# Performance work log

Hardware: AMD Instinct MI355X
Metric: run time of the kernel (lower is better)

Reference implementation:

```python
import jax, jax.numpy as jnp
import numpy as np

B, C, H, W = 4, 64, 128, 128
KS = 3
PAD = 1
N = KS * KS


def conv2d(x, w, b=None, stride=1, padding=0):
    out = jax.lax.conv_general_dilated(
        x, w, (stride, stride), [(padding, padding), (padding, padding)],
        dimension_numbers=("NCHW", "OIHW", "NCHW"))
    if b is not None:
        out = out + b[None, :, None, None]
    return out


def setup_inputs() -> dict:
    key = jax.random.key(0)
    ks = jax.random.split(key, 6)
    scale = 0.05  # small weights so offsets stay in a realistic range
    return {
        "x": jax.random.normal(ks[0], (B, C, H, W), jnp.float32),
        "p_w": jax.random.normal(ks[1], (2 * N, C, 3, 3), jnp.float32) * scale,
        "p_b": jax.random.normal(ks[2], (2 * N,), jnp.float32) * scale,
        "m_w": jax.random.normal(ks[3], (N, C, 3, 3), jnp.float32) * scale,
        "m_b": jax.random.normal(ks[4], (N,), jnp.float32) * scale,
        "conv_w": jax.random.normal(ks[5], (C, C, KS, KS), jnp.float32) * (1.0 / np.sqrt(C * N)),
    }


def reference(x, p_w, p_b, m_w, m_b, conv_w):
    b, c, h, w = x.shape
    # offset / modulation branches (stride=1, padding=1, 3x3)
    offset = conv2d(x, p_w, p_b, 1, 1)                 # (b, 2N, h, w)
    m = jax.nn.sigmoid(conv2d(x, m_w, m_b, 1, 1))      # (b, N,  h, w)

    xp = jnp.pad(x, ((0, 0), (0, 0), (PAD, PAD), (PAD, PAD)))
    Hp, Wp = h + 2 * PAD, w + 2 * PAD

    # sampling positions p = p_0 + p_n + offset, layout (b, h, w, 2N): first N rows(x), last N cols(y)
    pnx, pny = jnp.meshgrid(jnp.arange(-1, 2), jnp.arange(-1, 2), indexing="ij")
    p_n = jnp.concatenate([pnx.ravel(), pny.ravel()]).astype(x.dtype)          # (2N,)
    base_x = jnp.broadcast_to(jnp.arange(1, h + 1)[:, None, None], (h, w, N))
    base_y = jnp.broadcast_to(jnp.arange(1, w + 1)[None, :, None], (h, w, N))
    base = jnp.concatenate([base_x, base_y], axis=-1).astype(x.dtype)          # (h, w, 2N)
    p = jnp.transpose(offset, (0, 2, 3, 1)) + p_n + base[None]                 # (b, h, w, 2N)

    px, py = p[..., :N], p[..., N:]
    # integer corners from detached p (floor), clamped to padded extent
    qf = jnp.floor(jax.lax.stop_gradient(p))
    qx_lt = jnp.clip(qf[..., :N], 0, Hp - 1).astype(jnp.int32)
    qy_lt = jnp.clip(qf[..., N:], 0, Wp - 1).astype(jnp.int32)
    qx_rb = jnp.clip(qf[..., :N] + 1, 0, Hp - 1).astype(jnp.int32)
    qy_rb = jnp.clip(qf[..., N:] + 1, 0, Wp - 1).astype(jnp.int32)

    pxc = jnp.clip(px, 0, Hp - 1)
    pyc = jnp.clip(py, 0, Wp - 1)

    g_lt = (1 + (qx_lt - pxc)) * (1 + (qy_lt - pyc))
    g_rb = (1 - (qx_rb - pxc)) * (1 - (qy_rb - pyc))
    g_lb = (1 + (qx_lt - pxc)) * (1 - (qy_rb - pyc))
    g_rt = (1 - (qx_rb - pxc)) * (1 + (qy_lt - pyc))

    xp_flat = xp.reshape(b, c, Hp * Wp)

    def gather(qx, qy):
        idx = (qx * Wp + qy).reshape(b, -1)                     # (b, h*w*N)
        out = jax.vmap(lambda xf, i: xf[:, i])(xp_flat, idx)    # (b, c, h*w*N)
        return out.reshape(b, c, h, w, N)

    x_off = (g_lt[:, None] * gather(qx_lt, qy_lt)
             + g_rb[:, None] * gather(qx_rb, qy_rb)
             + g_lb[:, None] * gather(qx_lt, qy_rb)
             + g_rt[:, None] * gather(qx_rb, qy_lt))            # (b, c, h, w, N)

    x_off = x_off * jnp.transpose(m, (0, 2, 3, 1))[:, None]     # modulation

    # _reshape_x_offset: n = 3*i + j -> (b, c, h*3, w*3) with layout (h, i, w, j)
    x_off = x_off.reshape(b, c, h, w, KS, KS)
    x_off = jnp.transpose(x_off, (0, 1, 2, 4, 3, 5)).reshape(b, c, h * KS, w * KS)

    return conv2d(x_off, conv_w, None, stride=KS, padding=0)    # (b, outc, h, w)
```

## Files before the change

### kernel.cpp

```cpp
#include <hip/hip_runtime.h>
#include <hip/hip_bf16.h>
#include <math.h>

#define BB 4
#define CC 64
#define HH 128
#define WW 128
#define NPT 9
#define HW (HH*WW)
#define HP 130
#define WP 130

typedef __attribute__((ext_vector_type(8))) short bf16x8;
typedef __attribute__((ext_vector_type(4))) float f32x4;

static __device__ __forceinline__ unsigned short f2bf(float f) {
    __hip_bfloat16 h = __float2bfloat16(f);
    return *reinterpret_cast<unsigned short*>(&h);
}
static __device__ __forceinline__ float bf2f(unsigned short u) {
    return __uint_as_float(((unsigned int)u) << 16);
}

__global__ __launch_bounds__(256) void k_pre(
    const float* __restrict__ x, const float* __restrict__ cw,
    const float* __restrict__ pw, const float* __restrict__ pb,
    const float* __restrict__ mw, const float* __restrict__ mb,
    unsigned short* __restrict__ xt, unsigned short* __restrict__ wtt,
    unsigned short* __restrict__ wttB, float* __restrict__ b27)
{
    __shared__ float tile[64][132];
    int bid = blockIdx.x;
    int t = threadIdx.x;
    if (bid < BB * HH) {
        int b = bid >> 7, h = bid & 127;
        const float* xb = x + ((size_t)b * CC) * HW + h * WW;
        #pragma unroll
        for (int i = 0; i < 8; ++i) {
            int idx = i * 256 + t;
            int ci = idx >> 5, w4 = idx & 31;
            float4 v = *reinterpret_cast<const float4*>(xb + (size_t)ci * HW + w4 * 4);
            *reinterpret_cast<float4*>(&tile[ci][w4 * 4]) = v;
        }
        __syncthreads();
        unsigned short* xtb = xt + (((size_t)b * HP + (h + 1)) * WP + 1) * 64;
        #pragma unroll
        for (int i = 0; i < 4; ++i) {
            int idx = i * 256 + t;
            int w = idx >> 3, cig = idx & 7;
            unsigned int pk[4];
            #pragma unroll
            for (int k = 0; k < 4; ++k) {
                unsigned int u0 = f2bf(tile[cig * 8 + 2 * k][w]);
                unsigned int u1 = f2bf(tile[cig * 8 + 2 * k + 1][w]);
                pk[k] = u0 | (u1 << 16);
            }
            *reinterpret_cast<int4*>(xtb + (size_t)w * 64 + cig * 8) =
                *reinterpret_cast<int4*>(&pk[0]);
        }
        return;
    }
    int i = (bid - BB * HH) * 256 + t;
    if (i < 36864) {
        int cot = i / 9216;
        int rem = i - cot * 9216;
        int n   = rem >> 10;
        int s2  = (rem >> 9) & 1;
        int lhi = (rem >> 7) & 3;
        int l15 = (rem >> 3) & 15;
        int j   = i & 7;
        int co = cot * 16 + l15;
        int ci = s2 * 32 + lhi * 8 + j;
        wtt[i] = f2bf(cw[(co * 64 + ci) * 9 + n]);
    } else if (i < 55296) {
        int q = i - 36864;
        int j   = q & 7;
        int co  = (q >> 3) & 31;
        int lhi = (q >> 8) & 3;
        int s2  = (q >> 10) & 1;
        int n   = q >> 11;
        int ci  = s2 * 32 + lhi * 8 + j;
        float v = 0.f;
        if (co < 18) v = pw[(co * 64 + ci) * 9 + n];
        else if (co < 27) v = mw[((co - 18) * 64 + ci) * 9 + n];
        wttB[q] = f2bf(v);
    } else if (i < 55328) {
        int co = i - 55296;
        b27[co] = (co < 18) ? pb[co] : (co < 27 ? mb[co - 18] : 0.f);
    } else if (i < 55328 + BB * 4128) {
        int p = i - 55328;
        int b = p / 4128, r = p - b * 4128;
        size_t base;
        if (r < 2080) {
            int row = r / 1040;
            int rr  = r - row * 1040;
            int wp = rr >> 3, c8 = rr & 7;
            int hp = row ? (HP - 1) : 0;
            base = (((size_t)b * HP + hp) * WP + wp) * 64 + c8 * 8;
        } else {
            int r2 = r - 2080;
            int col = r2 >> 10;
            int rr  = r2 & 1023;
            int hp = (rr >> 3) + 1, c8 = rr & 7;
            int wp = col ? (WP - 1) : 0;
            base = (((size_t)b * HP + hp) * WP + wp) * 64 + c8 * 8;
        }
        *reinterpret_cast<int4*>(xt + base) = make_int4(0, 0, 0, 0);
    }
}

#define OMS 68
#define NCX 198

union SmemU {
    unsigned short astage[NCX * 64];
    struct {
        int geo[576 * 8];
        union {
            float om[27 * OMS];
            unsigned int xoff[2][2048];
        } u2;
    } d;
};

__global__ __launch_bounds__(512, 4) void k_fused(
    const unsigned short* __restrict__ xt, const unsigned short* __restrict__ wttB,
    const float* __restrict__ b27, const unsigned short* __restrict__ wtt,
    float* __restrict__ out)
{
    __shared__ SmemU su;

    int blk0 = blockIdx.x;
    int blk = (blk0 & 7) * 128 + (blk0 >> 3);
    int wblk = blk & 1;
    int h = (blk >> 1) & 127;
    int b = blk >> 8;
    int w0 = wblk * 64;
    int t = threadIdx.x;
    int ln = t & 63, wid = t >> 6;
    int ln15 = ln & 15, lhi = ln >> 4;

    const unsigned short* xtb = xt + (size_t)b * HP * WP * 64;
    char* astage_c = reinterpret_cast<char*>(su.astage);
    float* s_om = su.d.u2.om;

    for (int uu = t; uu < NCX * 8; uu += 512) {
        int cx = uu >> 3, o16 = uu & 7;
        int r = cx / 66, c = cx - r * 66;
        const unsigned short* src = xtb + ((size_t)(h + r) * WP + (w0 + c)) * 64 + o16 * 8;
        int4 v = *reinterpret_cast<const int4*>(src);
        *reinterpret_cast<int4*>(astage_c + cx * 128 + ((o16 ^ (cx & 7)) << 4)) = v;
    }
    __syncthreads();

    {
        int pxg = wid >> 1, coh = wid & 1;
        int px = pxg * 16 + ln15;
        f32x4 acc;
        acc[0] = 0.f; acc[1] = 0.f; acc[2] = 0.f; acc[3] = 0.f;
        const unsigned short* wB = wttB + (size_t)(coh * 16 + ln15) * 8 + lhi * 256;
        bf16x8 bfc = *reinterpret_cast<const bf16x8*>(wB);
        #pragma unroll
        for (int ns = 0; ns < 18; ++ns) {
            bf16x8 bfn = bfc;
            if (ns < 17)
                bfn = *reinterpret_cast<const bf16x8*>(wB + (size_t)(ns + 1) * 1024);
            int n = ns >> 1, s2 = ns & 1;
            int kh = n / 3, kw = n - kh * 3;
            int cx = kh * 66 + px + kw;
            int o16 = s2 * 4 + lhi;
            bf16x8 af = *reinterpret_cast<const bf16x8*>(
                astage_c + cx * 128 + ((o16 ^ (cx & 7)) << 4));
            acc = __builtin_amdgcn_mfma_f32_16x16x32_bf16(af, bfc, acc, 0, 0, 0);
            bfc = bfn;
        }
        __syncthreads();
        int co = coh * 16 + ln15;
        int prow = pxg * 16 + lhi * 4;
        if (co < 27) {
            float bias = b27[co];
            float4 v;
            v.x = acc[0] + bias; v.y = acc[1] + bias;
            v.z = acc[2] + bias; v.w = acc[3] + bias;
            if (co >= 18) {
                v.x = 1.f / (1.f + expf(-v.x));
                v.y = 1.f / (1.f + expf(-v.y));
                v.z = 1.f / (1.f + expf(-v.z));
                v.w = 1.f / (1.f + expf(-v.w));
            }
            *reinterpret_cast<float4*>(&s_om[co * OMS + prow]) = v;
        }
    }
    __syncthreads();

    int* s_geo = su.d.geo;

    for (int idx = t; idx < NPT * 64; idx += 512) {
        int n = idx >> 6, px = idx & 63;
        float ox = s_om[n * OMS + px];
        float oy = s_om[(9 + n) * OMS + px];
        float mk = s_om[(18 + n) * OMS + px];
        float pxf = ox + (float)(n / 3 - 1) + (float)(h + 1);
        float pyf = oy + (float)(n % 3 - 1) + (float)(w0 + px + 1);
        float fx = floorf(pxf), fy = floorf(pyf);
        int qxlt = (int)fminf(fmaxf(fx, 0.f), 129.f);
        int qylt = (int)fminf(fmaxf(fy, 0.f), 129.f);
        int qxrb = (int)fminf(fmaxf(fx + 1.f, 0.f), 129.f);
        int qyrb = (int)fminf(fmaxf(fy + 1.f, 0.f), 129.f);
        float pxc = fminf(fmaxf(pxf, 0.f), 129.f);
        float pyc = fminf(fmaxf(pyf, 0.f), 129.f);
        float ax = 1.f + (float)qxlt - pxc;
        float bx = 1.f - ((float)qxrb - pxc);
        float ay = 1.f + (float)qylt - pyc;
        float by = 1.f - ((float)qyrb - pyc);
        int* g = &s_geo[idx * 8];
        float4 wv;
        wv.x = ax * ay * mk;
        wv.y = bx * by * mk;
        wv.z = ax * by * mk;
        wv.w = bx * ay * mk;
        int4 av;
        av.x = (qxlt * WP + qylt) * 64;
        av.y = (qxrb * WP + qyrb) * 64;
        av.z = (qxlt * WP + qyrb) * 64;
        av.w = (qxrb * WP + qylt) * 64;
        *reinterpret_cast<float4*>(g) = wv;
        *reinterpret_cast<int4*>(g + 4) = av;
    }
    __syncthreads();

    f32x4 acc[2];
    #pragma unroll
    for (int g = 0; g < 2; ++g) {
        acc[g][0] = 0.f; acc[g][1] = 0.f; acc[g][2] = 0.f; acc[g][3] = 0.f;
    }

    const unsigned short* wbase = wtt + (size_t)(wid & 3) * 9216;
    int px_s = t >> 3;
    int cig_s = t & 7;
    int coff = cig_s * 8;
    char* xoff_base = reinterpret_cast<char*>(su.d.u2.xoff);
    int ghalf = wid >> 2;
    int wsw = (cig_s * 16) ^ ((px_s & 7) << 4);

    bf16x8 ga0, ga1, ga2, ga3, gb0, gb1, gb2, gb3;

#define GATHER(S0, S1, S2, S3, NN) do {                                        \
        const int4 av_ = *reinterpret_cast<const int4*>(                       \
            &s_geo[((NN) * 64 + px_s) * 8] + 4);                               \
        S0 = *reinterpret_cast<const bf16x8*>(xtb + av_.x + coff);             \
        S1 = *reinterpret_cast<const bf16x8*>(xtb + av_.y + coff);             \
        S2 = *reinterpret_cast<const bf16x8*>(xtb + av_.z + coff);             \
        S3 = *reinterpret_cast<const bf16x8*>(xtb + av_.w + coff);             \
    } while (0)

#define PACK(S0, S1, S2, S3, NN) do {                                          \
        const float4 wv_ = *reinterpret_cast<const float4*>(                   \
            &s_geo[((NN) * 64 + px_s) * 8]);                                   \
        unsigned int pk_[4];                                                   \
        _Pragma("unroll")                                                      \
        for (int i_ = 0; i_ < 4; ++i_) {                                       \
            float va_ = wv_.x * bf2f((unsigned short)S0[2*i_])                 \
                      + wv_.y * bf2f((unsigned short)S1[2*i_])                 \
                      + wv_.z * bf2f((unsigned short)S2[2*i_])                 \
                      + wv_.w * bf2f((unsigned short)S3[2*i_]);                \
            float vb_ = wv_.x * bf2f((unsigned short)S0[2*i_+1])               \
                      + wv_.y * bf2f((unsigned short)S1[2*i_+1])               \
                      + wv_.z * bf2f((unsigned short)S2[2*i_+1])               \
                      + wv_.w * bf2f((unsigned short)S3[2*i_+1]);              \
            pk_[i_] = __builtin_amdgcn_perm(__float_as_uint(vb_),              \
                                            __float_as_uint(va_), 0x07060302u); \
        }                                                                      \
        *reinterpret_cast<int4*>(xoff_base + ((NN) & 1) * 8192 + px_s * 128 + wsw) \
            = *reinterpret_cast<int4*>(&pk_[0]);                               \
    } while (0)

#define MFMA_N(NN) do {                                                        \
        bf16x8 bf0_ = *reinterpret_cast<const bf16x8*>(                        \
            wbase + (NN) * 1024 + lhi * 128 + ln15 * 8);                       \
        bf16x8 bf1_ = *reinterpret_cast<const bf16x8*>(                        \
            wbase + (NN) * 1024 + 512 + lhi * 128 + ln15 * 8);                 \
        char* rbuf_ = xoff_base + ((NN) & 1) * 8192;                           \
        _Pragma("unroll")                                                      \
        for (int s2_ = 0; s2_ < 2; ++s2_) {                                    \
            bf16x8 bfr_ = s2_ ? bf1_ : bf0_;                                   \
            _Pragma("unroll")                                                  \
            for (int g_ = 0; g_ < 2; ++g_) {                                   \
                int row_ = (ghalf * 2 + g_) * 16 + ln15;                       \
                int cb2_ = (s2_ * 32 + lhi * 8) * 2;                           \
                bf16x8 af_ = *reinterpret_cast<const bf16x8*>(                 \
                    rbuf_ + row_ * 128 + (cb2_ ^ ((row_ & 7) << 4)));          \
                acc[g_] = __builtin_amdgcn_mfma_f32_16x16x32_bf16(             \
                    af_, bfr_, acc[g_], 0, 0, 0);                              \
            }                                                                  \
        }                                                                      \
    } while (0)

    GATHER(ga0, ga1, ga2, ga3, 0);
    GATHER(gb0, gb1, gb2, gb3, 1);
    PACK(ga0, ga1, ga2, ga3, 0);
    __syncthreads();

#define DSTEP(NN, N0, N1, N2, N3, P0, P1, P2, P3) do {                         \
        if ((NN) + 2 < NPT) GATHER(N0, N1, N2, N3, (NN) + 2);                  \
        MFMA_N(NN);                                                            \
        if ((NN) + 1 < NPT) {                                                  \
            PACK(P0, P1, P2, P3, (NN) + 1);                                    \
            __syncthreads();                                                   \
        }                                                                      \
    } while (0)

    DSTEP(0, ga0, ga1, ga2, ga3, gb0, gb1, gb2, gb3);
    DSTEP(1, gb0, gb1, gb2, gb3, ga0, ga1, ga2, ga3);
    DSTEP(2, ga0, ga1, ga2, ga3, gb0, gb1, gb2, gb3);
    DSTEP(3, gb0, gb1, gb2, gb3, ga0, ga1, ga2, ga3);
    DSTEP(4, ga0, ga1, ga2, ga3, gb0, gb1, gb2, gb3);
    DSTEP(5, gb0, gb1, gb2, gb3, ga0, ga1, ga2, ga3);
    DSTEP(6, ga0, ga1, ga2, ga3, gb0, gb1, gb2, gb3);
    DSTEP(7, gb0, gb1, gb2, gb3, ga0, ga1, ga2, ga3);
    DSTEP(8, ga0, ga1, ga2, ga3, gb0, gb1, gb2, gb3);

    int co = (wid & 3) * 16 + ln15;
    float* orow = out + ((size_t)b * CC + co) * HW + h * WW + w0;
    #pragma unroll
    for (int g = 0; g < 2; ++g) {
        *reinterpret_cast<float4*>(orow + (ghalf * 2 + g) * 16 + lhi * 4) =
            *reinterpret_cast<float4*>(&acc[g]);
    }
}

extern "C" void kernel_launch(void* const* d_in, const int* in_sizes, int n_in,
                              void* d_out, int out_size, void* d_ws, size_t ws_size,
                              hipStream_t stream) {
    const float* x  = (const float*)d_in[0];
    const float* pw = (const float*)d_in[1];
    const float* pb = (const float*)d_in[2];
    const float* mw = (const float*)d_in[3];
    const float* mb = (const float*)d_in[4];
    const float* cw = (const float*)d_in[5];
    float* out = (float*)d_out;

    char* wsc = (char*)d_ws;
    unsigned short* xt  = (unsigned short*)wsc;
    size_t off = ((size_t)BB * HP * WP * 64 * 2 + 255) & ~(size_t)255;
    unsigned short* wtt = (unsigned short*)(wsc + off);
    off += (size_t)64 * 576 * 2;
    unsigned short* wttB = (unsigned short*)(wsc + off);
    off += (size_t)18432 * 2;
    float* b27 = (float*)(wsc + ((off + 255) & ~(size_t)255));

    int prep_items = 36864 + 18432 + 32 + BB * 4128;
    int prep_blocks = (prep_items + 255) / 256;
    hipLaunchKernelGGL(k_pre, dim3(BB * HH + prep_blocks), dim3(256), 0, stream,
                       x, cw, pw, pb, mw, mb, xt, wtt, wttB, b27);
    hipLaunchKernelGGL(k_fused, dim3(BB * HH * 2), dim3(512), 0, stream,
                       xt, wttB, b27, wtt, out);
}
```

Baseline: 40.45 us.

## Shrink fused block to 256 threads and build MFMA operands directly in registers

The fused deformable-conv kernel now runs 4 waves per block instead of 8. In the main loop each lane gathers and bilinearly blends the sampled pixels for its own row and feeds them straight into MFMA as the A operand. This removes the LDS staging buffer and the per-tap __syncthreads of the old double-buffered gather/pack/MFMA pipeline. Each wave now computes all 64 output channels for its 16 pixels, and the offset conv computes both channel halves per wave. In exchange it loses the explicit prefetch overlap of gathers with MFMA and uses more registers per thread.

```diff
diff --git a/kernel.cpp b/kernel.cpp
--- a/kernel.cpp
+++ b/kernel.cpp
@@ -116,14 +116,11 @@
     unsigned short astage[NCX * 64];
     struct {
         int geo[576 * 8];
-        union {
-            float om[27 * OMS];
-            unsigned int xoff[2][2048];
-        } u2;
+        float om[27 * OMS];
     } d;
 };
 
-__global__ __launch_bounds__(512, 4) void k_fused(
+__global__ __launch_bounds__(256, 4) void k_fused(
     const unsigned short* __restrict__ xt, const unsigned short* __restrict__ wttB,
     const float* __restrict__ b27, const unsigned short* __restrict__ wtt,
     float* __restrict__ out)
@@ -142,9 +139,9 @@
 
     const unsigned short* xtb = xt + (size_t)b * HP * WP * 64;
     char* astage_c = reinterpret_cast<char*>(su.astage);
-    float* s_om = su.d.u2.om;
-
-    for (int uu = t; uu < NCX * 8; uu += 512) {
+    float* s_om = su.d.om;
+
+    for (int uu = t; uu < NCX * 8; uu += 256) {
         int cx = uu >> 3, o16 = uu & 7;
         int r = cx / 66, c = cx - r * 66;
         const unsigned short* src = xtb + ((size_t)(h + r) * WP + (w0 + c)) * 64 + o16 * 8;
@@ -154,48 +151,56 @@
     __syncthreads();
 
     {
-        int pxg = wid >> 1, coh = wid & 1;
-        int px = pxg * 16 + ln15;
-        f32x4 acc;
-        acc[0] = 0.f; acc[1] = 0.f; acc[2] = 0.f; acc[3] = 0.f;
-        const unsigned short* wB = wttB + (size_t)(coh * 16 + ln15) * 8 + lhi * 256;
-        bf16x8 bfc = *reinterpret_cast<const bf16x8*>(wB);
+        int px = wid * 16 + ln15;
+        f32x4 a0, a1;
+        a0[0] = 0.f; a0[1] = 0.f; a0[2] = 0.f; a0[3] = 0.f;
+        a1 = a0;
         #pragma unroll
         for (int ns = 0; ns < 18; ++ns) {
-            bf16x8 bfn = bfc;
-            if (ns < 17)
-                bfn = *reinterpret_cast<const bf16x8*>(wB + (size_t)(ns + 1) * 1024);
             int n = ns >> 1, s2 = ns & 1;
             int kh = n / 3, kw = n - kh * 3;
             int cx = kh * 66 + px + kw;
             int o16 = s2 * 4 + lhi;
             bf16x8 af = *reinterpret_cast<const bf16x8*>(
                 astage_c + cx * 128 + ((o16 ^ (cx & 7)) << 4));
-            acc = __builtin_amdgcn_mfma_f32_16x16x32_bf16(af, bfc, acc, 0, 0, 0);
-            bfc = bfn;
+            bf16x8 b0 = *reinterpret_cast<const bf16x8*>(
+                wttB + ((size_t)(ns * 4 + lhi) * 32 + ln15) * 8);
+            bf16x8 b1 = *reinterpret_cast<const bf16x8*>(
+                wttB + ((size_t)(ns * 4 + lhi) * 32 + 16 + ln15) * 8);
+            a0 = __builtin_amdgcn_mfma_f32_16x16x32_bf16(af, b0, a0, 0, 0, 0);
+            a1 = __builtin_amdgcn_mfma_f32_16x16x32_bf16(af, b1, a1, 0, 0, 0);
         }
         __syncthreads();
-        int co = coh * 16 + ln15;
-        int prow = pxg * 16 + lhi * 4;
-        if (co < 27) {
-            float bias = b27[co];
+        int prow = wid * 16 + lhi * 4;
+        {
+            float bias = b27[ln15];
             float4 v;
-            v.x = acc[0] + bias; v.y = acc[1] + bias;
-            v.z = acc[2] + bias; v.w = acc[3] + bias;
-            if (co >= 18) {
-                v.x = 1.f / (1.f + expf(-v.x));
-                v.y = 1.f / (1.f + expf(-v.y));
-                v.z = 1.f / (1.f + expf(-v.z));
-                v.w = 1.f / (1.f + expf(-v.w));
+            v.x = a0[0] + bias; v.y = a0[1] + bias;
+            v.z = a0[2] + bias; v.w = a0[3] + bias;
+            *reinterpret_cast<float4*>(&s_om[ln15 * OMS + prow]) = v;
+        }
+        {
+            int co = 16 + ln15;
+            if (co < 27) {
+                float bias = b27[co];
+                float4 v;
+                v.x = a1[0] + bias; v.y = a1[1] + bias;
+                v.z = a1[2] + bias; v.w = a1[3] + bias;
+                if (co >= 18) {
+                    v.x = 1.f / (1.f + expf(-v.x));
+                    v.y = 1.f / (1.f + expf(-v.y));
+                    v.z = 1.f / (1.f + expf(-v.z));
+                    v.w = 1.f / (1.f + expf(-v.w));
+                }
+                *reinterpret_cast<float4*>(&s_om[co * OMS + prow]) = v;
             }
-            *reinterpret_cast<float4*>(&s_om[co * OMS + prow]) = v;
         }
     }
     __syncthreads();
 
     int* s_geo = su.d.geo;
 
-    for (int idx = t; idx < NPT * 64; idx += 512) {
+    for (int idx = t; idx < NPT * 64; idx += 256) {
         int n = idx >> 6, px = idx & 63;
         float ox = s_om[n * OMS + px];
         float oy = s_om[(9 + n) * OMS + px];
@@ -229,103 +234,63 @@
     }
     __syncthreads();
 
-    f32x4 acc[2];
+    f32x4 acc[4];
     #pragma unroll
-    for (int g = 0; g < 2; ++g) {
+    for (int g = 0; g < 4; ++g) {
         acc[g][0] = 0.f; acc[g][1] = 0.f; acc[g][2] = 0.f; acc[g][3] = 0.f;
     }
 
-    const unsigned short* wbase = wtt + (size_t)(wid & 3) * 9216;
-    int px_s = t >> 3;
-    int cig_s = t & 7;
-    int coff = cig_s * 8;
-    char* xoff_base = reinterpret_cast<char*>(su.d.u2.xoff);
-    int ghalf = wid >> 2;
-    int wsw = (cig_s * 16) ^ ((px_s & 7) << 4);
-
-    bf16x8 ga0, ga1, ga2, ga3, gb0, gb1, gb2, gb3;
-
-#define GATHER(S0, S1, S2, S3, NN) do {                                        \
-        const int4 av_ = *reinterpret_cast<const int4*>(                       \
-            &s_geo[((NN) * 64 + px_s) * 8] + 4);                               \
-        S0 = *reinterpret_cast<const bf16x8*>(xtb + av_.x + coff);             \
-        S1 = *reinterpret_cast<const bf16x8*>(xtb + av_.y + coff);             \
-        S2 = *reinterpret_cast<const bf16x8*>(xtb + av_.z + coff);             \
-        S3 = *reinterpret_cast<const bf16x8*>(xtb + av_.w + coff);             \
-    } while (0)
-
-#define PACK(S0, S1, S2, S3, NN) do {                                          \
-        const float4 wv_ = *reinterpret_cast<const float4*>(                   \
-            &s_geo[((NN) * 64 + px_s) * 8]);                                   \
-        unsigned int pk_[4];                                                   \
-        _Pragma("unroll")                                                      \
-        for (int i_ = 0; i_ < 4; ++i_) {                                       \
-            float va_ = wv_.x * bf2f((unsigned short)S0[2*i_])                 \
-                      + wv_.y * bf2f((unsigned short)S1[2*i_])                 \
-                      + wv_.z * bf2f((unsigned short)S2[2*i_])                 \
-                      + wv_.w * bf2f((unsigned short)S3[2*i_]);                \
-            float vb_ = wv_.x * bf2f((unsigned short)S0[2*i_+1])               \
-                      + wv_.y * bf2f((unsigned short)S1[2*i_+1])               \
-                      + wv_.z * bf2f((unsigned short)S2[2*i_+1])               \
-                      + wv_.w * bf2f((unsigned short)S3[2*i_+1]);              \
-            pk_[i_] = __builtin_amdgcn_perm(__float_as_uint(vb_),              \
-                                            __float_as_uint(va_), 0x07060302u); \
-        }                                                                      \
-        *reinterpret_cast<int4*>(xoff_base + ((NN) & 1) * 8192 + px_s * 128 + wsw) \
-            = *reinterpret_cast<int4*>(&pk_[0]);                               \
-    } while (0)
-
-#define MFMA_N(NN) do {                                                        \
-        bf16x8 bf0_ = *reinterpret_cast<const bf16x8*>(                        \
-            wbase + (NN) * 1024 + lhi * 128 + ln15 * 8);                       \
-        bf16x8 bf1_ = *reinterpret_cast<const bf16x8*>(                        \
-            wbase + (NN) * 1024 + 512 + lhi * 128 + ln15 * 8);                 \
-        char* rbuf_ = xoff_base + ((NN) & 1) * 8192;                           \
-        _Pragma("unroll")                                                      \
-        for (int s2_ = 0; s2_ < 2; ++s2_) {                                    \
-            bf16x8 bfr_ = s2_ ? bf1_ : bf0_;                                   \
-            _Pragma("unroll")                                                  \
-            for (int g_ = 0; g_ < 2; ++g_) {                                   \
-                int row_ = (ghalf * 2 + g_) * 16 + ln15;                       \
-                int cb2_ = (s2_ * 32 + lhi * 8) * 2;                           \
-                bf16x8 af_ = *reinterpret_cast<const bf16x8*>(                 \
-                    rbuf_ + row_ * 128 + (cb2_ ^ ((row_ & 7) << 4)));          \
-                acc[g_] = __builtin_amdgcn_mfma_f32_16x16x32_bf16(             \
-                    af_, bfr_, acc[g_], 0, 0, 0);                              \
-            }                                                                  \
-        }                                                                      \
-    } while (0)
-
-    GATHER(ga0, ga1, ga2, ga3, 0);
-    GATHER(gb0, gb1, gb2, gb3, 1);
-    PACK(ga0, ga1, ga2, ga3, 0);
-    __syncthreads();
-
-#define DSTEP(NN, N0, N1, N2, N3, P0, P1, P2, P3) do {                         \
-        if ((NN) + 2 < NPT) GATHER(N0, N1, N2, N3, (NN) + 2);                  \
-        MFMA_N(NN);                                                            \
-        if ((NN) + 1 < NPT) {                                                  \
-            PACK(P0, P1, P2, P3, (NN) + 1);                                    \
-            __syncthreads();                                                   \
-        }                                                                      \
-    } while (0)
-
-    DSTEP(0, ga0, ga1, ga2, ga3, gb0, gb1, gb2, gb3);
-    DSTEP(1, gb0, gb1, gb2, gb3, ga0, ga1, ga2, ga3);
-    DSTEP(2, ga0, ga1, ga2, ga3, gb0, gb1, gb2, gb3);
-    DSTEP(3, gb0, gb1, gb2, gb3, ga0, ga1, ga2, ga3);
-    DSTEP(4, ga0, ga1, ga2, ga3, gb0, gb1, gb2, gb3);
-    DSTEP(5, gb0, gb1, gb2, gb3, ga0, ga1, ga2, ga3);
-    DSTEP(6, ga0, ga1, ga2, ga3, gb0, gb1, gb2, gb3);
-    DSTEP(7, gb0, gb1, gb2, gb3, ga0, ga1, ga2, ga3);
-    DSTEP(8, ga0, ga1, ga2, ga3, gb0, gb1, gb2, gb3);
-
-    int co = (wid & 3) * 16 + ln15;
-    float* orow = out + ((size_t)b * CC + co) * HW + h * WW + w0;
+    int c0off = lhi * 8;
+    int c1off = 32 + lhi * 8;
+    const int* mygeo = &s_geo[(wid * 16 + ln15) * 8];
+
+    for (int n = 0; n < NPT; ++n) {
+        const float4 wv = *reinterpret_cast<const float4*>(mygeo + n * 512);
+        const int4  av = *reinterpret_cast<const int4*>(mygeo + n * 512 + 4);
+
+        bf16x8 c00 = *reinterpret_cast<const bf16x8*>(xtb + av.x + c0off);
+        bf16x8 c10 = *reinterpret_cast<const bf16x8*>(xtb + av.y + c0off);
+        bf16x8 c20 = *reinterpret_cast<const bf16x8*>(xtb + av.z + c0off);
+        bf16x8 c30 = *reinterpret_cast<const bf16x8*>(xtb + av.w + c0off);
+        bf16x8 c01 = *reinterpret_cast<const bf16x8*>(xtb + av.x + c1off);
+        bf16x8 c11 = *reinterpret_cast<const bf16x8*>(xtb + av.y + c1off);
+        bf16x8 c21 = *reinterpret_cast<const bf16x8*>(xtb + av.z + c1off);
+        bf16x8 c31 = *reinterpret_cast<const bf16x8*>(xtb + av.w + c1off);
+
+        unsigned int p0[4], p1[4];
+        #pragma unroll
+        for (int i = 0; i < 4; ++i) {
+            float va0 = wv.x * bf2f((unsigned short)c00[2*i])   + wv.y * bf2f((unsigned short)c10[2*i])
+                      + wv.z * bf2f((unsigned short)c20[2*i])   + wv.w * bf2f((unsigned short)c30[2*i]);
+            float vb0 = wv.x * bf2f((unsigned short)c00[2*i+1]) + wv.y * bf2f((unsigned short)c10[2*i+1])
+                      + wv.z * bf2f((unsigned short)c20[2*i+1]) + wv.w * bf2f((unsigned short)c30[2*i+1]);
+            p0[i] = __builtin_amdgcn_perm(__float_as_uint(vb0), __float_as_uint(va0), 0x07060302u);
+            float va1 = wv.x * bf2f((unsigned short)c01[2*i])   + wv.y * bf2f((unsigned short)c11[2*i])
+                      + wv.z * bf2f((unsigned short)c21[2*i])   + wv.w * bf2f((unsigned short)c31[2*i]);
+            float vb1 = wv.x * bf2f((unsigned short)c01[2*i+1]) + wv.y * bf2f((unsigned short)c11[2*i+1])
+                      + wv.z * bf2f((unsigned short)c21[2*i+1]) + wv.w * bf2f((unsigned short)c31[2*i+1]);
+            p1[i] = __builtin_amdgcn_perm(__float_as_uint(vb1), __float_as_uint(va1), 0x07060302u);
+        }
+        bf16x8 af0 = *reinterpret_cast<bf16x8*>(&p0[0]);
+        bf16x8 af1 = *reinterpret_cast<bf16x8*>(&p1[0]);
+
+        #pragma unroll
+        for (int cot = 0; cot < 4; ++cot) {
+            bf16x8 bf0 = *reinterpret_cast<const bf16x8*>(
+                wtt + (size_t)cot * 9216 + n * 1024 + lhi * 128 + ln15 * 8);
+            bf16x8 bf1 = *reinterpret_cast<const bf16x8*>(
+                wtt + (size_t)cot * 9216 + n * 1024 + 512 + lhi * 128 + ln15 * 8);
+            acc[cot] = __builtin_amdgcn_mfma_f32_16x16x32_bf16(af0, bf0, acc[cot], 0, 0, 0);
+            acc[cot] = __builtin_amdgcn_mfma_f32_16x16x32_bf16(af1, bf1, acc[cot], 0, 0, 0);
+        }
+    }
+
     #pragma unroll
-    for (int g = 0; g < 2; ++g) {
-        *reinterpret_cast<float4*>(orow + (ghalf * 2 + g) * 16 + lhi * 4) =
-            *reinterpret_cast<float4*>(&acc[g]);
+    for (int cot = 0; cot < 4; ++cot) {
+        int co = cot * 16 + ln15;
+        float* orow = out + ((size_t)b * CC + co) * HW + h * WW + w0;
+        *reinterpret_cast<float4*>(orow + wid * 16 + lhi * 4) =
+            *reinterpret_cast<float4*>(&acc[cot]);
     }
 }
 
@@ -353,6 +318,6 @@
     int prep_blocks = (prep_items + 255) / 256;
     hipLaunchKernelGGL(k_pre, dim3(BB * HH + prep_blocks), dim3(256), 0, stream,
                        x, cw, pw, pb, mw, mb, xt, wtt, wttB, b27);
-    hipLaunchKernelGGL(k_fused, dim3(BB * HH * 2), dim3(512), 0, stream,
+    hipLaunchKernelGGL(k_fused, dim3(BB * HH * 2), dim3(256), 0, stream,
                        xt, wttB, b27, wtt, out);
 }
```

New measurement: 62.06 us. 53.4% more time.
